# Optimization experiments

Hardware: AMD Instinct MI355X
Metric: run time of the kernel (lower is better)

The kernel has to match this reference:

```python
import jax, jax.numpy as jnp
import numpy as np

B, T, D, H = 32, 4096, 512, 512


def setup_inputs() -> dict:
    key = jax.random.key(0)
    ks = jax.random.split(key, 8)
    s = 1.0 / np.sqrt(D)
    return {
        "hidden_state": jax.random.normal(ks[0], (B, D), jnp.float32),
        "encoder_outputs": jax.random.normal(ks[1], (B, T, D), jnp.float32),
        "W": jax.random.normal(ks[2], (D, H), jnp.float32) * s,
        "U": jax.random.normal(ks[3], (D, H), jnp.float32) * s,
        "V": jax.random.normal(ks[4], (H,), jnp.float32) * s,
        "bias": jnp.zeros((H,), jnp.float32),
        "Wa": jax.random.normal(ks[5], (H, H), jnp.float32) * (1.0 / np.sqrt(H)),
        "ba": jnp.zeros((H,), jnp.float32),
    }


def reference(hidden_state, encoder_outputs, W, U, V, bias, Wa, ba):
    # dens1: [B,1,H] ; dens2: [B,T,H]
    dens1 = jnp.einsum('bd,dh->bh', hidden_state, W)[:, None, :]
    dens2 = jnp.einsum('btd,dh->bth', encoder_outputs, U)
    pre = dens1 + dens2 + bias                       # [B,T,H]
    tanh_ = jnp.tanh(jnp.einsum('bth,hk->btk', pre, Wa) + ba)  # extra Dense(tanh)
    cij = jnp.einsum('bth,h->bt', tanh_, V)          # [B,T]
    alphas = jax.nn.softmax(cij, axis=-1)            # [B,T]
    output = jnp.einsum('btd,bt->bd', encoder_outputs, alphas)  # weighted sum
    return output, alphas
```

## Files before the change

### kernel.cpp

```cpp
#include <hip/hip_runtime.h>
#include <hip/hip_bf16.h>


#define BB 32
#define TT 4096
#define DD 512
#define HH 512
#define BK 64

typedef short s16x8 __attribute__((ext_vector_type(8)));
typedef float f32x4 __attribute__((ext_vector_type(4)));

union FU { float f; unsigned u; };

static __device__ __forceinline__ unsigned pack_bf16_trunc(float a, float b) {
    FU ua, ub; ua.f = a; ub.f = b;
    return (ua.u >> 16) | (ub.u & 0xffff0000u);
}

static __device__ __forceinline__ unsigned short f2bf_rne(float x) {
    FU v; v.f = x;
    unsigned u = v.u;
    u = u + 0x7fffu + ((u >> 16) & 1u);
    return (unsigned short)(u >> 16);
}

static __device__ __forceinline__ float tanh_fast(float x) {
    float e = __expf(2.0f * x);
    return 1.0f - 2.0f * __builtin_amdgcn_rcpf(e + 1.0f);
}

static __device__ __forceinline__ void gload_lds16(const void* g, void* l) {
    __builtin_amdgcn_global_load_lds(
        (const __attribute__((address_space(1))) unsigned int*)g,
        (__attribute__((address_space(3))) unsigned int*)l, 16, 0, 0);
}

__global__ void k_dens1(const float* __restrict__ hs, const float* __restrict__ W,
                        const float* __restrict__ bias, float* __restrict__ g) {
    int bi = blockIdx.x;
    int dc = bi & 3, hb = (bi >> 2) & 1, b = bi >> 3;
    int h = hb * 256 + threadIdx.x;
    float s = (dc == 0) ? bias[h] : 0.0f;
    int d0 = dc * 128;
    #pragma unroll 4
    for (int d = 0; d < 128; ++d)
        s = fmaf(hs[b * DD + d0 + d], W[(size_t)(d0 + d) * HH + h], s);
    atomicAdd(&g[b * HH + h], s);
}

__global__ void k_cvec(const float* __restrict__ g, const float* __restrict__ Wa,
                       const float* __restrict__ ba, float* __restrict__ cvec) {
    int bi = blockIdx.x;
    int hc = bi & 3, kb = (bi >> 2) & 1, b = bi >> 3;
    int k = kb * 256 + threadIdx.x;
    float s = (hc == 0) ? ba[k] : 0.0f;
    int h0 = hc * 128;
    #pragma unroll 4
    for (int h = 0; h < 128; ++h)
        s = fmaf(g[b * HH + h0 + h], Wa[(size_t)(h0 + h) * HH + k], s);
    atomicAdd(&cvec[b * HH + k], s);
}

__global__ void k_uwa(const float* __restrict__ U, const float* __restrict__ Wa,
                      unsigned short* __restrict__ UWaT) {
    int d0 = blockIdx.x * 8;
    int tid = threadIdx.x;
    __shared__ float Us[8][DD];
    #pragma unroll
    for (int i = 0; i < 16; ++i) {
        int idx = i * 256 + tid;
        Us[idx >> 9][idx & 511] = U[(size_t)(d0 + (idx >> 9)) * HH + (idx & 511)];
    }
    __syncthreads();
    float acc[8][2] = {};
    #pragma unroll 2
    for (int h = 0; h < DD; ++h) {
        float w0 = Wa[(size_t)h * HH + tid];
        float w1 = Wa[(size_t)h * HH + 256 + tid];
        #pragma unroll
        for (int dd = 0; dd < 8; ++dd) {
            float u = Us[dd][h];
            acc[dd][0] = fmaf(u, w0, acc[dd][0]);
            acc[dd][1] = fmaf(u, w1, acc[dd][1]);
        }
    }
    #pragma unroll
    for (int dd = 0; dd < 8; ++dd) {
        UWaT[(size_t)tid * DD + d0 + dd] = f2bf_rne(acc[dd][0]);
        UWaT[(size_t)(tid + 256) * DD + d0 + dd] = f2bf_rne(acc[dd][1]);
    }
}

__global__ void __launch_bounds__(256, 2) k_gemm_tanh(
    const float* __restrict__ e, const unsigned short* __restrict__ Bt,
    const float* __restrict__ cvec, const float* __restrict__ V,
    float* __restrict__ cij) {
    int tid = threadIdx.x;
    int m0 = blockIdx.x * 64;
    int lane = tid & 63, w = tid >> 6;
    int wn = w * 128;
    int lcol = lane & 15, q = lane >> 4;
    int rl = lane >> 3, gg = lane & 7;

    __shared__ __align__(16) unsigned short As[64 * BK];
    __shared__ __align__(16) unsigned short Bs[512 * BK];

    f32x4 acc[4][8] = {};

    const float* Abase = e + (size_t)m0 * DD;

    for (int k0 = 0; k0 < DD; k0 += BK) {
        float4 av[4];
        #pragma unroll
        for (int it = 0; it < 4; ++it) {
            int idx = it * 256 + tid;
            int row = idx >> 4, c4 = idx & 15;
            av[it] = *(const float4*)(Abase + (size_t)row * DD + k0 + c4 * 4);
        }
        #pragma unroll
        for (int u = 0; u < 16; ++u) {
            int n0 = w * 128 + u * 8;
            const unsigned short* gp =
                Bt + (size_t)(n0 + rl) * DD + k0 + ((gg ^ rl) << 3);
            gload_lds16(gp, &Bs[n0 * 64]);
        }
        #pragma unroll
        for (int it = 0; it < 4; ++it) {
            int idx = it * 256 + tid;
            int row = idx >> 4, c4 = idx & 15;
            uint2 wv;
            wv.x = pack_bf16_trunc(av[it].x, av[it].y);
            wv.y = pack_bf16_trunc(av[it].z, av[it].w);
            int g = c4 >> 1, half = c4 & 1;
            *(uint2*)&As[(g * 64 + (row ^ g)) * 8 + half * 4] = wv;
        }
        __syncthreads();
        #pragma unroll
        for (int ks = 0; ks < BK; ks += 32) {
            int gk = ks >> 3;
            s16x8 af[4], bfr[8];
            #pragma unroll
            for (int i = 0; i < 4; ++i) {
                int row = i * 16 + lcol, g = gk + q;
                af[i] = *(const s16x8*)&As[(g * 64 + (row ^ g)) * 8];
            }
            #pragma unroll
            for (int j = 0; j < 8; ++j) {
                int col = wn + j * 16 + lcol, g = gk + q;
                bfr[j] = *(const s16x8*)&Bs[col * 64 + ((g ^ (col & 7)) << 3)];
            }
            #pragma unroll
            for (int i = 0; i < 4; ++i)
                #pragma unroll
                for (int j = 0; j < 8; ++j)
                    acc[i][j] = __builtin_amdgcn_mfma_f32_16x16x32_bf16(
                        af[i], bfr[j], acc[i][j], 0, 0, 0);
        }
        __syncthreads();
    }

    int b = m0 >> 12;
    float cvv[8], Vv[8];
    #pragma unroll
    for (int j = 0; j < 8; ++j) {
        int h = wn + j * 16 + lcol;
        cvv[j] = cvec[b * HH + h];
        Vv[j] = V[h];
    }
    #pragma unroll
    for (int i = 0; i < 4; ++i) {
        #pragma unroll
        for (int r = 0; r < 4; ++r) {
            float s = 0.0f;
            #pragma unroll
            for (int j = 0; j < 8; ++j)
                s = fmaf(tanh_fast(acc[i][j][r] + cvv[j]), Vv[j], s);
            s += __shfl_xor(s, 1);
            s += __shfl_xor(s, 2);
            s += __shfl_xor(s, 4);
            s += __shfl_xor(s, 8);
            if (lcol == 0)
                atomicAdd(&cij[m0 + i * 16 + q * 4 + r], s);
        }
    }
}

__global__ void k_softmax(const float* __restrict__ cij, float* __restrict__ alphas) {
    int b = blockIdx.x, tid = threadIdx.x;
    const float* row = cij + (size_t)b * TT;
    __shared__ float red[4];
    float m = -1e30f;
    for (int t = tid; t < TT; t += 256) m = fmaxf(m, row[t]);
    #pragma unroll
    for (int o = 1; o < 64; o <<= 1) m = fmaxf(m, __shfl_xor(m, o));
    if ((tid & 63) == 0) red[tid >> 6] = m;
    __syncthreads();
    m = fmaxf(fmaxf(red[0], red[1]), fmaxf(red[2], red[3]));
    __syncthreads();
    float sum = 0.0f;
    for (int t = tid; t < TT; t += 256) sum += __expf(row[t] - m);
    #pragma unroll
    for (int o = 1; o < 64; o <<= 1) sum += __shfl_xor(sum, o);
    if ((tid & 63) == 0) red[tid >> 6] = sum;
    __syncthreads();
    float inv = 1.0f / (red[0] + red[1] + red[2] + red[3]);
    for (int t = tid; t < TT; t += 256)
        alphas[(size_t)b * TT + t] = __expf(row[t] - m) * inv;
}

__global__ void k_wsum(const float* __restrict__ e, const float* __restrict__ alphas,
                       float* __restrict__ pw) {
    int b = blockIdx.x >> 6;
    int chunk = blockIdx.x & 63;
    int t0 = chunk * 64;
    int tid = threadIdx.x;
    int half = tid >> 7, f4 = tid & 127;
    const float* base = e + (size_t)b * TT * DD;
    const float* al = alphas + (size_t)b * TT;
    f32x4 a0 = {0, 0, 0, 0}, a1 = {0, 0, 0, 0};
    for (int it = 0; it < 16; ++it) {
        int t = t0 + it * 4 + half;
        float w0 = al[t], w1 = al[t + 2];
        f32x4 v0 = *(const f32x4*)(base + (size_t)t * DD + f4 * 4);
        f32x4 v1 = *(const f32x4*)(base + (size_t)(t + 2) * DD + f4 * 4);
        a0 += w0 * v0;
        a1 += w1 * v1;
    }
    a0 += a1;
    __shared__ f32x4 red[128];
    if (half == 1) red[f4] = a0;
    __syncthreads();
    if (half == 0) {
        a0 += red[f4];
        *(f32x4*)&pw[((size_t)(b * 64 + chunk)) * DD + f4 * 4] = a0;
    }
}

__global__ void k_wred(const float* __restrict__ pw, float* __restrict__ out) {
    int b = blockIdx.x, tid = threadIdx.x;
    float2 acc = {0.0f, 0.0f};
    const float* base = pw + (size_t)b * 64 * DD;
    #pragma unroll 4
    for (int c = 0; c < 64; ++c) {
        float2 v = *(const float2*)(base + (size_t)c * DD + tid * 2);
        acc.x += v.x;
        acc.y += v.y;
    }
    *(float2*)&out[b * DD + tid * 2] = acc;
}

extern "C" void kernel_launch(void* const* d_in, const int* in_sizes, int n_in,
                              void* d_out, int out_size, void* d_ws, size_t ws_size,
                              hipStream_t stream) {
    const float* hs   = (const float*)d_in[0];
    const float* e    = (const float*)d_in[1];
    const float* W    = (const float*)d_in[2];
    const float* U    = (const float*)d_in[3];
    const float* V    = (const float*)d_in[4];
    const float* bias = (const float*)d_in[5];
    const float* Wa   = (const float*)d_in[6];
    const float* ba   = (const float*)d_in[7];

    float* out    = (float*)d_out;
    float* alphas = out + BB * DD;

    float*          cij  = (float*)d_ws;
    float*          g    = (float*)((char*)d_ws + 524288);
    float*          cvec = (float*)((char*)d_ws + 589824);
    unsigned short* Bt   = (unsigned short*)((char*)d_ws + 655360);
    float*          pw   = (float*)((char*)d_ws + 1179648);

    hipMemsetAsync(d_ws, 0, 655360, stream);

    k_dens1<<<256, 256, 0, stream>>>(hs, W, bias, g);
    k_cvec<<<256, 256, 0, stream>>>(g, Wa, ba, cvec);
    k_uwa<<<64, 256, 0, stream>>>(U, Wa, Bt);
    k_gemm_tanh<<<2048, 256, 0, stream>>>(e, Bt, cvec, V, cij);
    k_softmax<<<BB, 256, 0, stream>>>(cij, alphas);
    k_wsum<<<BB * 64, 256, 0, stream>>>(e, alphas, pw);
    k_wred<<<BB, 256, 0, stream>>>(pw, out);
}
```

Before: 567.7 us.

## Fuse prep kernels, prefetch A tiles, drop atomics and memset, unroll wsum

Merges the dens1, cvec and U·Wa precompute kernels into one launch and removes the workspace memset. The GEMM now prefetches the next A tile into registers while MFMAs run. It also replaces the per-row atomicAdd into cij with an LDS reduction across the four waves followed by a plain store. The weighted-sum kernel gains more independent accumulators for memory-level parallelism. These changes target launch overhead, atomic traffic and load latency, but the fused prep runs the per-batch matvec serially within only 32 blocks and the prefetch raises register pressure.

```diff
diff --git a/kernel.cpp b/kernel.cpp
--- a/kernel.cpp
+++ b/kernel.cpp
@@ -36,59 +36,65 @@
         (__attribute__((address_space(3))) unsigned int*)l, 16, 0, 0);
 }
 
-__global__ void k_dens1(const float* __restrict__ hs, const float* __restrict__ W,
-                        const float* __restrict__ bias, float* __restrict__ g) {
+__global__ void k_prep(const float* __restrict__ hs, const float* __restrict__ W,
+                       const float* __restrict__ bias, const float* __restrict__ Wa,
+                       const float* __restrict__ ba, const float* __restrict__ U,
+                       float* __restrict__ cvec, unsigned short* __restrict__ UWaT) {
     int bi = blockIdx.x;
-    int dc = bi & 3, hb = (bi >> 2) & 1, b = bi >> 3;
-    int h = hb * 256 + threadIdx.x;
-    float s = (dc == 0) ? bias[h] : 0.0f;
-    int d0 = dc * 128;
-    #pragma unroll 4
-    for (int d = 0; d < 128; ++d)
-        s = fmaf(hs[b * DD + d0 + d], W[(size_t)(d0 + d) * HH + h], s);
-    atomicAdd(&g[b * HH + h], s);
-}
-
-__global__ void k_cvec(const float* __restrict__ g, const float* __restrict__ Wa,
-                       const float* __restrict__ ba, float* __restrict__ cvec) {
-    int bi = blockIdx.x;
-    int hc = bi & 3, kb = (bi >> 2) & 1, b = bi >> 3;
-    int k = kb * 256 + threadIdx.x;
-    float s = (hc == 0) ? ba[k] : 0.0f;
-    int h0 = hc * 128;
-    #pragma unroll 4
-    for (int h = 0; h < 128; ++h)
-        s = fmaf(g[b * HH + h0 + h], Wa[(size_t)(h0 + h) * HH + k], s);
-    atomicAdd(&cvec[b * HH + k], s);
-}
-
-__global__ void k_uwa(const float* __restrict__ U, const float* __restrict__ Wa,
-                      unsigned short* __restrict__ UWaT) {
-    int d0 = blockIdx.x * 8;
     int tid = threadIdx.x;
-    __shared__ float Us[8][DD];
-    #pragma unroll
-    for (int i = 0; i < 16; ++i) {
-        int idx = i * 256 + tid;
-        Us[idx >> 9][idx & 511] = U[(size_t)(d0 + (idx >> 9)) * HH + (idx & 511)];
-    }
-    __syncthreads();
-    float acc[8][2] = {};
-    #pragma unroll 2
-    for (int h = 0; h < DD; ++h) {
-        float w0 = Wa[(size_t)h * HH + tid];
-        float w1 = Wa[(size_t)h * HH + 256 + tid];
+    __shared__ float sm[8 * DD];
+    if (bi < 32) {
+        int b = bi;
+        float* hsb = sm;
+        float* gs = sm + DD;
+        hsb[tid] = hs[b * DD + tid];
+        hsb[tid + 256] = hs[b * DD + tid + 256];
+        __syncthreads();
+        float a0 = bias[tid], a1 = bias[tid + 256];
+        #pragma unroll 4
+        for (int d = 0; d < DD; ++d) {
+            float h = hsb[d];
+            a0 = fmaf(h, W[(size_t)d * HH + tid], a0);
+            a1 = fmaf(h, W[(size_t)d * HH + tid + 256], a1);
+        }
+        gs[tid] = a0;
+        gs[tid + 256] = a1;
+        __syncthreads();
+        float c0 = ba[tid], c1 = ba[tid + 256];
+        #pragma unroll 4
+        for (int h = 0; h < HH; ++h) {
+            float g = gs[h];
+            c0 = fmaf(g, Wa[(size_t)h * HH + tid], c0);
+            c1 = fmaf(g, Wa[(size_t)h * HH + tid + 256], c1);
+        }
+        cvec[b * HH + tid] = c0;
+        cvec[b * HH + tid + 256] = c1;
+    } else {
+        int d0 = (bi - 32) * 8;
+        float (*Us)[DD] = (float (*)[DD])sm;
+        #pragma unroll
+        for (int i = 0; i < 16; ++i) {
+            int idx = i * 256 + tid;
+            Us[idx >> 9][idx & 511] = U[(size_t)(d0 + (idx >> 9)) * HH + (idx & 511)];
+        }
+        __syncthreads();
+        float acc[8][2] = {};
+        #pragma unroll 2
+        for (int h = 0; h < DD; ++h) {
+            float w0 = Wa[(size_t)h * HH + tid];
+            float w1 = Wa[(size_t)h * HH + 256 + tid];
+            #pragma unroll
+            for (int dd = 0; dd < 8; ++dd) {
+                float u = Us[dd][h];
+                acc[dd][0] = fmaf(u, w0, acc[dd][0]);
+                acc[dd][1] = fmaf(u, w1, acc[dd][1]);
+            }
+        }
         #pragma unroll
         for (int dd = 0; dd < 8; ++dd) {
-            float u = Us[dd][h];
-            acc[dd][0] = fmaf(u, w0, acc[dd][0]);
-            acc[dd][1] = fmaf(u, w1, acc[dd][1]);
-        }
-    }
-    #pragma unroll
-    for (int dd = 0; dd < 8; ++dd) {
-        UWaT[(size_t)tid * DD + d0 + dd] = f2bf_rne(acc[dd][0]);
-        UWaT[(size_t)(tid + 256) * DD + d0 + dd] = f2bf_rne(acc[dd][1]);
+            UWaT[(size_t)tid * DD + d0 + dd] = f2bf_rne(acc[dd][0]);
+            UWaT[(size_t)(tid + 256) * DD + d0 + dd] = f2bf_rne(acc[dd][1]);
+        }
     }
 }
 
@@ -108,16 +114,22 @@
 
     f32x4 acc[4][8] = {};
 
+    int arow[4], ac4[4];
+    #pragma unroll
+    for (int it = 0; it < 4; ++it) {
+        int idx = it * 256 + tid;
+        arow[it] = idx >> 4;
+        ac4[it] = idx & 15;
+    }
     const float* Abase = e + (size_t)m0 * DD;
 
+    float4 av[4];
+    #pragma unroll
+    for (int it = 0; it < 4; ++it)
+        av[it] = *(const float4*)(Abase + (size_t)arow[it] * DD + ac4[it] * 4);
+
     for (int k0 = 0; k0 < DD; k0 += BK) {
-        float4 av[4];
-        #pragma unroll
-        for (int it = 0; it < 4; ++it) {
-            int idx = it * 256 + tid;
-            int row = idx >> 4, c4 = idx & 15;
-            av[it] = *(const float4*)(Abase + (size_t)row * DD + k0 + c4 * 4);
-        }
+        if (k0) __syncthreads();
         #pragma unroll
         for (int u = 0; u < 16; ++u) {
             int n0 = w * 128 + u * 8;
@@ -127,15 +139,19 @@
         }
         #pragma unroll
         for (int it = 0; it < 4; ++it) {
-            int idx = it * 256 + tid;
-            int row = idx >> 4, c4 = idx & 15;
             uint2 wv;
             wv.x = pack_bf16_trunc(av[it].x, av[it].y);
             wv.y = pack_bf16_trunc(av[it].z, av[it].w);
-            int g = c4 >> 1, half = c4 & 1;
-            *(uint2*)&As[(g * 64 + (row ^ g)) * 8 + half * 4] = wv;
-        }
-        __syncthreads();
+            int g = ac4[it] >> 1, half = ac4[it] & 1;
+            *(uint2*)&As[(g * 64 + (arow[it] ^ g)) * 8 + half * 4] = wv;
+        }
+        __syncthreads();
+        if (k0 < DD - BK) {
+            #pragma unroll
+            for (int it = 0; it < 4; ++it)
+                av[it] = *(const float4*)(Abase + (size_t)arow[it] * DD +
+                                          (k0 + BK) + ac4[it] * 4);
+        }
         #pragma unroll
         for (int ks = 0; ks < BK; ks += 32) {
             int gk = ks >> 3;
@@ -157,9 +173,10 @@
                     acc[i][j] = __builtin_amdgcn_mfma_f32_16x16x32_bf16(
                         af[i], bfr[j], acc[i][j], 0, 0, 0);
         }
-        __syncthreads();
-    }
-
+    }
+
+    __syncthreads();
+    float* red = (float*)As;
     int b = m0 >> 12;
     float cvv[8], Vv[8];
     #pragma unroll
@@ -181,9 +198,12 @@
             s += __shfl_xor(s, 4);
             s += __shfl_xor(s, 8);
             if (lcol == 0)
-                atomicAdd(&cij[m0 + i * 16 + q * 4 + r], s);
-        }
-    }
+                red[w * 64 + i * 16 + q * 4 + r] = s;
+        }
+    }
+    __syncthreads();
+    if (tid < 64)
+        cij[m0 + tid] = red[tid] + red[64 + tid] + red[128 + tid] + red[192 + tid];
 }
 
 __global__ void k_softmax(const float* __restrict__ cij, float* __restrict__ alphas) {
@@ -213,21 +233,20 @@
                        float* __restrict__ pw) {
     int b = blockIdx.x >> 6;
     int chunk = blockIdx.x & 63;
-    int t0 = chunk * 64;
     int tid = threadIdx.x;
     int half = tid >> 7, f4 = tid & 127;
-    const float* base = e + (size_t)b * TT * DD;
-    const float* al = alphas + (size_t)b * TT;
-    f32x4 a0 = {0, 0, 0, 0}, a1 = {0, 0, 0, 0};
-    for (int it = 0; it < 16; ++it) {
-        int t = t0 + it * 4 + half;
-        float w0 = al[t], w1 = al[t + 2];
-        f32x4 v0 = *(const f32x4*)(base + (size_t)t * DD + f4 * 4);
-        f32x4 v1 = *(const f32x4*)(base + (size_t)(t + 2) * DD + f4 * 4);
-        a0 += w0 * v0;
-        a1 += w1 * v1;
-    }
-    a0 += a1;
+    const float* base = e + (size_t)b * TT * DD + (size_t)chunk * 64 * DD + f4 * 4;
+    const float* al = alphas + (size_t)b * TT + chunk * 64;
+    f32x4 a0 = {0,0,0,0}, a1 = {0,0,0,0}, a2 = {0,0,0,0}, a3 = {0,0,0,0};
+    for (int it = 0; it < 8; ++it) {
+        int t = it * 8 + half;
+        float w0 = al[t], w1 = al[t + 2], w2 = al[t + 4], w3 = al[t + 6];
+        a0 += w0 * *(const f32x4*)(base + (size_t)t * DD);
+        a1 += w1 * *(const f32x4*)(base + (size_t)(t + 2) * DD);
+        a2 += w2 * *(const f32x4*)(base + (size_t)(t + 4) * DD);
+        a3 += w3 * *(const f32x4*)(base + (size_t)(t + 6) * DD);
+    }
+    a0 += a1; a2 += a3; a0 += a2;
     __shared__ f32x4 red[128];
     if (half == 1) red[f4] = a0;
     __syncthreads();
@@ -266,16 +285,12 @@
     float* alphas = out + BB * DD;
 
     float*          cij  = (float*)d_ws;
-    float*          g    = (float*)((char*)d_ws + 524288);
-    float*          cvec = (float*)((char*)d_ws + 589824);
-    unsigned short* Bt   = (unsigned short*)((char*)d_ws + 655360);
+    float*          cvec = (float*)((char*)d_ws + 524288);
+    unsigned short* Bt   = (unsigned short*)((char*)d_ws + 589824);
     float*          pw   = (float*)((char*)d_ws + 1179648);
 
-    hipMemsetAsync(d_ws, 0, 655360, stream);
-
-    k_dens1<<<256, 256, 0, stream>>>(hs, W, bias, g);
-    k_cvec<<<256, 256, 0, stream>>>(g, Wa, ba, cvec);
-    k_uwa<<<64, 256, 0, stream>>>(U, Wa, Bt);
+
+    k_prep<<<96, 256, 0, stream>>>(hs, W, bias, Wa, ba, U, cvec, Bt);
     k_gemm_tanh<<<2048, 256, 0, stream>>>(e, Bt, cvec, V, cij);
     k_softmax<<<BB, 256, 0, stream>>>(cij, alphas);
     k_wsum<<<BB * 64, 256, 0, stream>>>(e, alphas, pw);
```

Result: no change. 569.6 us (+0.3%).
